# Optimization experiments

Measured on AMD Instinct MI355X. Metric: run time of the kernel, lower is better.

## Reference

```python
import jax, jax.numpy as jnp
import numpy as np

EPS = 1e-5


def _conv3x3(x, w):
    # x: [B,C,H,W], w: [O,I,3,3], stride 1, padding 1
    return jax.lax.conv_general_dilated(
        x, w, window_strides=(1, 1), padding=((1, 1), (1, 1)),
        dimension_numbers=("NCHW", "OIHW", "NCHW"))


def _bn(x, g, b, m, v):
    # inference-mode BatchNorm2d over channel dim
    inv = jax.lax.rsqrt(v + EPS) * g
    return x * inv[None, :, None, None] + (b - m * inv)[None, :, None, None]


def setup_inputs() -> dict:
    key = jax.random.key(0)
    B, C, H, W = 32, 256, 56, 56
    ks = jax.random.split(key, 16)
    x = jax.random.normal(ks[0], (B, C, H, W), dtype=jnp.float32)
    mask = (jax.random.uniform(ks[1], (B, 1, H, W)) < 0.5).astype(jnp.float32)
    # dilated mask = 3x3 max-pool of mask
    mask_dilate = jax.lax.reduce_window(
        mask, -jnp.inf, jax.lax.max, (1, 1, 3, 3), (1, 1, 1, 1), "SAME")
    mask_dilate = jnp.maximum(mask_dilate, 0.0).astype(jnp.float32)
    vector = (jax.random.uniform(ks[2], (B, C)) < 0.5).astype(jnp.float32)
    conv1_w = jax.random.normal(ks[3], (C, C, 3, 3), dtype=jnp.float32) * 0.05
    conv2_w = jax.random.normal(ks[4], (C, C, 3, 3), dtype=jnp.float32) * 0.05
    bn1_g = 1.0 + 0.1 * jax.random.normal(ks[5], (C,), dtype=jnp.float32)
    bn1_b = 0.1 * jax.random.normal(ks[6], (C,), dtype=jnp.float32)
    bn1_m = 0.1 * jax.random.normal(ks[7], (C,), dtype=jnp.float32)
    bn1_v = 0.5 + jax.random.uniform(ks[8], (C,), dtype=jnp.float32)
    bn2_g = 1.0 + 0.1 * jax.random.normal(ks[9], (C,), dtype=jnp.float32)
    bn2_b = 0.1 * jax.random.normal(ks[10], (C,), dtype=jnp.float32)
    bn2_m = 0.1 * jax.random.normal(ks[11], (C,), dtype=jnp.float32)
    bn2_v = 0.5 + jax.random.uniform(ks[12], (C,), dtype=jnp.float32)
    return dict(x=x, mask=mask, mask_dilate=mask_dilate, vector=vector,
                conv1_w=conv1_w, bn1_g=bn1_g, bn1_b=bn1_b, bn1_m=bn1_m, bn1_v=bn1_v,
                conv2_w=conv2_w, bn2_g=bn2_g, bn2_b=bn2_b, bn2_m=bn2_m, bn2_v=bn2_v)


def reference(x, mask, mask_dilate, vector,
              conv1_w, bn1_g, bn1_b, bn1_m, bn1_v,
              conv2_w, bn2_g, bn2_b, bn2_m, bn2_v):
    # Sparse BasicBlock, stride=1, no downsample, input_mask=True.
    identity = x
    h = x * mask_dilate                      # apply_mask(x, mask_dilate)
    h = _conv3x3(h, conv1_w) * mask          # conv3x3_mask(conv1, ...)
    h = jax.nn.relu(_bn(h, bn1_g, bn1_b, bn1_m, bn1_v)) * mask_dilate  # bn_relu_mask(bn1, relu, ., mask_dilate)
    h = h * mask                             # apply_mask(x, mask)
    h = h * vector[:, :, None, None]         # channel_process(x, vector)
    h = _conv3x3(h, conv2_w) * mask          # conv3x3_mask(conv2, ...)
    h = _bn(h, bn2_g, bn2_b, bn2_m, bn2_v) * mask  # bn_relu_mask(bn2, None, ., mask)
    out = identity + h * mask                # identity + apply_mask(x, mask)
    return jax.nn.relu(out)
```

## Files before the change

### kernel.cpp

```cpp
#include <hip/hip_runtime.h>
#include <cstdint>


#define EPS 1e-5f

constexpr int Bn = 32, Cc = 256, Hh = 56, Ww = 56;
constexpr int HW = Hh * Ww;
constexpr int PD = 58;
constexpr int PP = PD * PD;
constexpr int SLAB = PP * 8;
constexpr int IMG_ELEMS = 32 * SLAB;
constexpr int WP_ELEMS = 2 * 16 * 9 * 2 * 128 * 8;

typedef __bf16 bf16x8 __attribute__((ext_vector_type(8)));
typedef float  f32x16 __attribute__((ext_vector_type(16)));

__global__ void pack_xm(const float* __restrict__ x, const float* __restrict__ md,
                        __bf16* __restrict__ xm) {
    int prow = blockIdx.x, img = blockIdx.y;
    int gy = prow - 1;
    bool rv = (unsigned)gy < 56u;
    for (int u = threadIdx.x; u < 32 * 64; u += 256) {
        int cg = u >> 6, pcol = u & 63;
        if (pcol >= PD) continue;
        int gx = pcol - 1;
        bf16x8 v = {};
        if (rv && (unsigned)gx < 56u) {
            float mdv = md[img * HW + gy * 56 + gx];
            const float* xp = x + ((size_t)img * Cc + cg * 8) * HW + gy * 56 + gx;
            #pragma unroll
            for (int j = 0; j < 8; ++j)
                v[j] = (__bf16)(xp[(size_t)j * HW] * mdv);
        }
        *(bf16x8*)&xm[(size_t)(img * 32 + cg) * SLAB + (prow * PD + pcol) * 8] = v;
    }
}

__global__ void cmap_kern(const float* __restrict__ vec, int* __restrict__ act,
                          int* __restrict__ inv, int* __restrict__ meta) {
    int img = threadIdx.x;
    if (img >= Bn) return;
    int n = 0;
    for (int c = 0; c < Cc; ++c) {
        if (vec[img * Cc + c] != 0.f) { act[img * Cc + n] = c; inv[img * Cc + c] = n; ++n; }
        else inv[img * Cc + c] = -1;
    }
    for (int k = n; k < Cc; ++k) act[img * Cc + k] = 0;
    meta[img] = n;
    meta[Bn + img] = (n + 15) >> 4;
}

__global__ void zero_u(__bf16* __restrict__ u, const int* __restrict__ meta) {
    int img = blockIdx.x;
    int nact = meta[img], nch = meta[Bn + img];
    __bf16* base = u + (size_t)img * IMG_ELEMS;
    bf16x8 z = {};
    int nslab = 2 * nch;
    for (int s = 0; s < nslab; ++s) {
        __bf16* sb = base + (size_t)s * SLAB;
        if (8 * s + 7 >= nact) {
            for (int t = threadIdx.x; t < PP; t += 256)
                *(bf16x8*)&sb[t * 8] = z;
        } else {
            for (int t = threadIdx.x; t < 228; t += 256) {
                int prow, pcol;
                if (t < 58)       { prow = 0;        pcol = t; }
                else if (t < 116) { prow = 57;       pcol = t - 58; }
                else if (t < 172) { prow = t - 115;  pcol = 0; }
                else              { prow = t - 171;  pcol = 57; }
                *(bf16x8*)&sb[(prow * PD + pcol) * 8] = z;
            }
        }
    }
}

__global__ void pack_w1(const float* __restrict__ w1, __bf16* __restrict__ wp1) {
    int id = blockIdx.x * 256 + threadIdx.x;
    int j = id & 7; int t = id >> 3;
    int col = t & 127; t >>= 7;
    int half = t & 1; t >>= 1;
    int tap = t % 9; t /= 9;
    int chunk = t & 15; int coblk = t >> 4;
    int co = coblk * 128 + col;
    int ci = chunk * 16 + half * 8 + j;
    wp1[id] = (__bf16)(w1[((size_t)co * Cc + ci) * 9 + tap]);
}

__global__ void gather_w2(const float* __restrict__ w2, const int* __restrict__ act,
                          const int* __restrict__ meta, __bf16* __restrict__ wp2g) {
    int img = blockIdx.y;
    int id = blockIdx.x * 256 + threadIdx.x;
    int nact = meta[img], nch = meta[Bn + img];
    int j = id & 7; int t = id >> 3;
    int col = t & 127; t >>= 7;
    int half = t & 1; t >>= 1;
    int tap = t % 9; t /= 9;
    int chunk = t & 15; int coblk = t >> 4;
    if (chunk >= nch) return;
    int kslot = chunk * 16 + half * 8 + j;
    float v = 0.f;
    if (kslot < nact) {
        int co = coblk * 128 + col;
        v = w2[((size_t)co * Cc + act[img * Cc + kslot]) * 9 + tap];
    }
    wp2g[(size_t)img * WP_ELEMS + id] = (__bf16)v;
}

__global__ void bn_prep(const float* g1, const float* b1, const float* m1, const float* v1,
                        const float* g2, const float* b2, const float* m2, const float* v2,
                        float* binv1, float* bbeta1, float* binv2, float* bbeta2) {
    int c = threadIdx.x;
    float i1 = g1[c] * rsqrtf(v1[c] + EPS);
    binv1[c] = i1; bbeta1[c] = b1[c] - m1[c] * i1;
    float i2 = g2[c] * rsqrtf(v2[c] + EPS);
    binv2[c] = i2; bbeta2[c] = b2[c] - m2[c] * i2;
}

__device__ __forceinline__ void gl_lds16(const __bf16* g, __bf16* l) {
    __builtin_amdgcn_global_load_lds(
        (const __attribute__((address_space(1))) void*)g,
        (__attribute__((address_space(3))) void*)l, 16, 0, 0);
}

template <bool C1>
__global__ __launch_bounds__(256, 3)
void conv_kern(const __bf16* __restrict__ src,
               const __bf16* __restrict__ wp,
               const float* __restrict__ maskg,
               const float* __restrict__ vec,
               const int* __restrict__ inv,
               const int* __restrict__ meta,
               const float* __restrict__ binv, const float* __restrict__ bbeta,
               const float* __restrict__ xin,
               void* __restrict__ dstv) {
    constexpr int SINB = 2 * 4 * 66 * 8;
    constexpr int SWB  = 9 * 2 * 128 * 8;
    __shared__ __align__(16) __bf16 s_in[SINB];
    __shared__ __align__(16) __bf16 s_w[SWB];

    const int tid = threadIdx.x;
    const int lane = tid & 63, wave = tid >> 6;
    const int xlane = lane & 31, halfid = lane >> 5;
    const int pxg = wave >> 1, cog = wave & 1;

    const int bid = blockIdx.x;
    const int wg = (bid & 7) * 224 + (bid >> 3);
    const int img = wg / 56;
    const int t = wg - img * 56;
    const int y0 = (t >> 1) * 2;
    const int coblk = t & 1;
    const int co0c = coblk * 128;

    const int nloop = C1 ? 16 : meta[Bn + img];

    f32x16 acc[2][2];
    #pragma unroll
    for (int a = 0; a < 2; ++a)
        #pragma unroll
        for (int b = 0; b < 2; ++b)
            #pragma unroll
            for (int r = 0; r < 16; ++r) acc[a][b][r] = 0.f;

    const __bf16* wblk = C1 ? (wp + (size_t)coblk * (16 * SWB))
                            : (wp + (size_t)img * WP_ELEMS + (size_t)coblk * (16 * SWB));
    const float* maskp = maskg + (size_t)img * HW;
    const __bf16* srcimg = src + (size_t)img * IMG_ELEMS;

    auto STAGE_IN = [&](int chunk) {
        const __bf16* slab = srcimg + (size_t)chunk * (2 * SLAB);
        #pragma unroll
        for (int k = 0; k < 3; ++k) {
            int u0 = wave * 64 + k * 256;
            int u = u0 + lane;
            if (u < 528) {
                int half = u / 264, rem = u - half * 264;
                int row = rem / 66, xx = rem - row * 66;
                int pcol = xx < PD ? xx : PD - 1;
                gl_lds16(slab + ((size_t)half * SLAB) + ((y0 + row) * PD + pcol) * 8,
                         &s_in[u0 * 8]);
            }
        }
    };
    auto STAGE_W = [&](int chunk) {
        const __bf16* g = wblk + (size_t)chunk * SWB;
        #pragma unroll
        for (int k = 0; k < 9; ++k) {
            int u0 = wave * 64 + k * 256;
            gl_lds16(g + (size_t)(u0 + lane) * 8, &s_w[u0 * 8]);
        }
    };

    for (int c = 0; c < nloop; ++c) {
        STAGE_W(c);
        STAGE_IN(c);
        asm volatile("s_waitcnt vmcnt(0)" ::: "memory");
        __builtin_amdgcn_sched_barrier(0);
        __builtin_amdgcn_s_barrier();
        __builtin_amdgcn_sched_barrier(0);

        __builtin_amdgcn_s_setprio(1);
        #pragma unroll
        for (int kh = 0; kh < 3; ++kh)
            #pragma unroll
            for (int kw = 0; kw < 3; ++kw) {
                const int tap = kh * 3 + kw;
                bf16x8 wf[2], inf[2];
                #pragma unroll
                for (int jt = 0; jt < 2; ++jt)
                    wf[jt] = *(const bf16x8*)&s_w[((tap * 2 + halfid) * 128 +
                                                   (cog * 2 + jt) * 32 + xlane) * 8];
                #pragma unroll
                for (int it = 0; it < 2; ++it) {
                    int yy = pxg + kh;
                    int xx = it * 32 + xlane + kw;
                    inf[it] = *(const bf16x8*)&s_in[((halfid * 4 + yy) * 66 + xx) * 8];
                }
                #pragma unroll
                for (int it = 0; it < 2; ++it)
                    #pragma unroll
                    for (int jt = 0; jt < 2; ++jt) {
                        if constexpr (C1)
                            acc[it][jt] = __builtin_amdgcn_mfma_f32_32x32x16_bf16(
                                inf[it], wf[jt], acc[it][jt], 0, 0, 0);
                        else
                            acc[it][jt] = __builtin_amdgcn_mfma_f32_32x32x16_bf16(
                                wf[jt], inf[it], acc[it][jt], 0, 0, 0);
                    }
            }
        __builtin_amdgcn_s_setprio(0);
        __builtin_amdgcn_sched_barrier(0);
        __builtin_amdgcn_s_barrier();
        __builtin_amdgcn_sched_barrier(0);
    }

    const int y = y0 + pxg;
    if constexpr (C1) {
        __bf16* u = (__bf16*)dstv;
        float iv[2], bt[2], vv[2]; int slt[2]; size_t slb[2];
        #pragma unroll
        for (int jt = 0; jt < 2; ++jt) {
            int co = co0c + (cog * 2 + jt) * 32 + xlane;
            iv[jt] = binv[co];
            bt[jt] = bbeta[co];
            vv[jt] = vec[img * Cc + co];
            slt[jt] = inv[img * Cc + co];
            int s = slt[jt] < 0 ? 0 : slt[jt];
            slb[jt] = (size_t)(img * 32 + (s >> 3)) * SLAB + (s & 7);
        }
        #pragma unroll
        for (int it = 0; it < 2; ++it) {
            int xb = it * 32;
            #pragma unroll
            for (int reg = 0; reg < 16; ++reg) {
                int x = xb + (reg & 3) + 8 * (reg >> 2) + 4 * halfid;
                if (x < 56) {
                    float mv = maskp[y * 56 + x];
                    int poff = ((y + 1) * PD + (x + 1)) * 8;
                    #pragma unroll
                    for (int jt = 0; jt < 2; ++jt) {
                        if (slt[jt] >= 0) {
                            float o = fmaxf(fmaf(acc[it][jt][reg], iv[jt], bt[jt]), 0.f)
                                      * mv * vv[jt];
                            u[slb[jt] + poff] = (__bf16)o;
                        }
                    }
                }
            }
        }
    } else {
        float* outp = (float*)dstv;
        int xa[2]; float mva[2]; bool ok[2];
        #pragma unroll
        for (int it = 0; it < 2; ++it) {
            xa[it] = it * 32 + xlane;
            ok[it] = xa[it] < 56;
            mva[it] = ok[it] ? maskp[y * 56 + xa[it]] : 0.f;
        }
        #pragma unroll
        for (int jt = 0; jt < 2; ++jt) {
            int cb = co0c + (cog * 2 + jt) * 32;
            #pragma unroll
            for (int rg = 0; rg < 4; ++rg) {
                int c4 = cb + 8 * rg + 4 * halfid;
                float4 iv4 = *(const float4*)&binv[c4];
                float4 bt4 = *(const float4*)&bbeta[c4];
                float ivv[4] = {iv4.x, iv4.y, iv4.z, iv4.w};
                float btv[4] = {bt4.x, bt4.y, bt4.z, bt4.w};
                #pragma unroll
                for (int j = 0; j < 4; ++j) {
                    int reg = rg * 4 + j;
                    int co = c4 + j;
                    size_t cbase = (size_t)(img * Cc + co) * HW;
                    #pragma unroll
                    for (int it = 0; it < 2; ++it) {
                        if (ok[it]) {
                            size_t oa = cbase + y * 56 + xa[it];
                            float ov = fmaxf(
                                xin[oa] + mva[it] * fmaf(acc[it][jt][reg], ivv[j], btv[j]),
                                0.f);
                            outp[oa] = ov;
                        }
                    }
                }
            }
        }
    }
}

extern "C" void kernel_launch(void* const* d_in, const int* in_sizes, int n_in,
                              void* d_out, int out_size, void* d_ws, size_t ws_size,
                              hipStream_t stream) {
    const float* x    = (const float*)d_in[0];
    const float* mask = (const float*)d_in[1];
    const float* md   = (const float*)d_in[2];
    const float* vec  = (const float*)d_in[3];
    const float* w1   = (const float*)d_in[4];
    const float* bn1g = (const float*)d_in[5];
    const float* bn1b = (const float*)d_in[6];
    const float* bn1m = (const float*)d_in[7];
    const float* bn1v = (const float*)d_in[8];
    const float* w2   = (const float*)d_in[9];
    const float* bn2g = (const float*)d_in[10];
    const float* bn2b = (const float*)d_in[11];
    const float* bn2m = (const float*)d_in[12];
    const float* bn2v = (const float*)d_in[13];
    float* out = (float*)d_out;

    const size_t npad = (size_t)Bn * IMG_ELEMS;
    __bf16* xm  = (__bf16*)d_ws;
    __bf16* u   = xm + npad;
    __bf16* wp1 = u + npad;
    int* act    = (int*)(wp1 + WP_ELEMS);
    int* invm   = act + Bn * Cc;
    int* meta   = invm + Bn * Cc;
    float* binv1  = (float*)(meta + 64);
    float* bbeta1 = binv1 + 256;
    float* binv2  = bbeta1 + 256;
    float* bbeta2 = binv2 + 256;
    __bf16* wp2g = xm;

    pack_xm<<<dim3(PD, Bn), dim3(256), 0, stream>>>(x, md, xm);
    pack_w1<<<dim3(WP_ELEMS / 256), dim3(256), 0, stream>>>(w1, wp1);
    cmap_kern<<<dim3(1), dim3(64), 0, stream>>>(vec, act, invm, meta);
    zero_u<<<dim3(Bn), dim3(256), 0, stream>>>(u, meta);
    bn_prep<<<dim3(1), dim3(256), 0, stream>>>(bn1g, bn1b, bn1m, bn1v,
                                               bn2g, bn2b, bn2m, bn2v,
                                               binv1, bbeta1, binv2, bbeta2);

    conv_kern<true><<<dim3(1792), dim3(256), 0, stream>>>(
        xm, wp1, mask, vec, invm, meta, binv1, bbeta1, nullptr, u);
    gather_w2<<<dim3(WP_ELEMS / 256, Bn), dim3(256), 0, stream>>>(w2, act, meta, wp2g);
    conv_kern<false><<<dim3(1792), dim3(256), 0, stream>>>(
        u, wp2g, mask, nullptr, invm, meta, binv2, bbeta2, x, out);
}
```

Measured before the change: 569.0 us.

## Skip inactive output channels in conv1 via per-image gathered weights

Conv1 now computes only the output channels that are active in the channel vector. A new per-image gather packs the active channels' weights into compact slots, and a block whose 128-channel tile is entirely inactive exits early, so with about half the channels active roughly half the conv1 blocks skip their MFMA work. Conv2's weight gather reads from a pre-transposed bf16 copy and writes vectorized 8-element chunks, and the channel-map kernel uses wavefront ballots across one block per image. In exchange there are extra gather and transpose kernels, the output buffer is used as scratch for the gathered conv1 weights, and per-image weight reads replace shared ones, which can lower cache reuse.

```diff
diff --git a/kernel.cpp b/kernel.cpp
--- a/kernel.cpp
+++ b/kernel.cpp
@@ -37,17 +37,21 @@
 }
 
 __global__ void cmap_kern(const float* __restrict__ vec, int* __restrict__ act,
-                          int* __restrict__ inv, int* __restrict__ meta) {
-    int img = threadIdx.x;
-    if (img >= Bn) return;
-    int n = 0;
-    for (int c = 0; c < Cc; ++c) {
-        if (vec[img * Cc + c] != 0.f) { act[img * Cc + n] = c; inv[img * Cc + c] = n; ++n; }
-        else inv[img * Cc + c] = -1;
-    }
-    for (int k = n; k < Cc; ++k) act[img * Cc + k] = 0;
-    meta[img] = n;
-    meta[Bn + img] = (n + 15) >> 4;
+                          int* __restrict__ meta) {
+    int img = blockIdx.x, lane = threadIdx.x;
+    int base = 0;
+    #pragma unroll
+    for (int g = 0; g < 4; ++g) {
+        int c = g * 64 + lane;
+        bool a = vec[img * Cc + c] != 0.f;
+        unsigned long long m = __ballot(a);
+        int pos = __popcll(m & ((1ull << lane) - 1ull));
+        if (a) act[img * Cc + base + pos] = c;
+        base += (int)__popcll(m);
+    }
+    __syncthreads();
+    for (int k = base + lane; k < Cc; k += 64) act[img * Cc + k] = 0;
+    if (lane == 0) { meta[img] = base; meta[Bn + img] = (base + 15) >> 4; }
 }
 
 __global__ void zero_u(__bf16* __restrict__ u, const int* __restrict__ meta) {
@@ -86,24 +90,57 @@
     wp1[id] = (__bf16)(w1[((size_t)co * Cc + ci) * 9 + tap]);
 }
 
-__global__ void gather_w2(const float* __restrict__ w2, const int* __restrict__ act,
-                          const int* __restrict__ meta, __bf16* __restrict__ wp2g) {
+__global__ void pack_w2T(const float* __restrict__ w2, __bf16* __restrict__ wpT) {
+    int id = blockIdx.x * 256 + threadIdx.x;
+    int co = id & 255; int t = id >> 8;
+    int tap = t % 9; int ci = t / 9;
+    wpT[id] = (__bf16)(w2[((size_t)co * Cc + ci) * 9 + tap]);
+}
+
+__global__ void gather_w1(const __bf16* __restrict__ wp1, const int* __restrict__ act,
+                          const int* __restrict__ meta, __bf16* __restrict__ wp1g) {
     int img = blockIdx.y;
-    int id = blockIdx.x * 256 + threadIdx.x;
-    int nact = meta[img], nch = meta[Bn + img];
-    int j = id & 7; int t = id >> 3;
-    int col = t & 127; t >>= 7;
+    int uidx = blockIdx.x * 256 + threadIdx.x;
+    int nact = meta[img];
+    int col = uidx & 127; int t = uidx >> 7;
     int half = t & 1; t >>= 1;
     int tap = t % 9; t /= 9;
     int chunk = t & 15; int coblk = t >> 4;
+    if (coblk * 128 >= nact) return;
+    int slot = coblk * 128 + col;
+    bf16x8 v = {};
+    if (slot < nact) {
+        int co = act[img * Cc + slot];
+        v = *(const bf16x8*)&wp1[(size_t)(((((co >> 7) * 16 + chunk) * 9 + tap) * 2 + half)
+                                          * 128 + (co & 127)) * 8];
+    }
+    *(bf16x8*)&wp1g[(size_t)img * WP_ELEMS + (size_t)uidx * 8] = v;
+}
+
+__global__ void gather_w2(const __bf16* __restrict__ wpT, const int* __restrict__ act,
+                          const int* __restrict__ meta, __bf16* __restrict__ wp2g) {
+    int img = blockIdx.y;
+    int blk = blockIdx.x;
+    int coblk = blk >> 4, chunk = blk & 15;
+    int nact = meta[img], nch = meta[Bn + img];
     if (chunk >= nch) return;
-    int kslot = chunk * 16 + half * 8 + j;
-    float v = 0.f;
-    if (kslot < nact) {
-        int co = coblk * 128 + col;
-        v = w2[((size_t)co * Cc + act[img * Cc + kslot]) * 9 + tap];
-    }
-    wp2g[(size_t)img * WP_ELEMS + id] = (__bf16)v;
+    int half = threadIdx.x >> 7, co = threadIdx.x & 127;
+    int cog = coblk * 128 + co;
+    int ci8[8];
+    #pragma unroll
+    for (int j = 0; j < 8; ++j) {
+        int ks = chunk * 16 + half * 8 + j;
+        ci8[j] = ks < nact ? act[img * Cc + ks] : -1;
+    }
+    #pragma unroll
+    for (int tap = 0; tap < 9; ++tap) {
+        bf16x8 v;
+        #pragma unroll
+        for (int j = 0; j < 8; ++j)
+            v[j] = ci8[j] >= 0 ? wpT[(size_t)(ci8[j] * 9 + tap) * 256 + cog] : (__bf16)0.f;
+        *(bf16x8*)&wp2g[(size_t)img * WP_ELEMS +
+                        (size_t)((((coblk * 16 + chunk) * 9 + tap) * 2 + half) * 128 + co) * 8] = v;
+    }
 }
 
 __global__ void bn_prep(const float* g1, const float* b1, const float* m1, const float* v1,
@@ -127,8 +164,7 @@
 void conv_kern(const __bf16* __restrict__ src,
                const __bf16* __restrict__ wp,
                const float* __restrict__ maskg,
-               const float* __restrict__ vec,
-               const int* __restrict__ inv,
+               const int* __restrict__ act,
                const int* __restrict__ meta,
                const float* __restrict__ binv, const float* __restrict__ bbeta,
                const float* __restrict__ xin,
@@ -151,6 +187,8 @@
     const int coblk = t & 1;
     const int co0c = coblk * 128;
 
+    const int nact = meta[img];
+    if constexpr (C1) { if (co0c >= nact) return; }
     const int nloop = C1 ? 16 : meta[Bn + img];
 
     f32x16 acc[2][2];
@@ -161,8 +199,7 @@
             #pragma unroll
             for (int r = 0; r < 16; ++r) acc[a][b][r] = 0.f;
 
-    const __bf16* wblk = C1 ? (wp + (size_t)coblk * (16 * SWB))
-                            : (wp + (size_t)img * WP_ELEMS + (size_t)coblk * (16 * SWB));
+    const __bf16* wblk = wp + (size_t)img * WP_ELEMS + (size_t)coblk * (16 * SWB);
     const float* maskp = maskg + (size_t)img * HW;
     const __bf16* srcimg = src + (size_t)img * IMG_ELEMS;
 
@@ -236,16 +273,15 @@
     const int y = y0 + pxg;
     if constexpr (C1) {
         __bf16* u = (__bf16*)dstv;
-        float iv[2], bt[2], vv[2]; int slt[2]; size_t slb[2];
+        float iv[2], bt[2]; bool on[2]; size_t slb[2];
         #pragma unroll
         for (int jt = 0; jt < 2; ++jt) {
-            int co = co0c + (cog * 2 + jt) * 32 + xlane;
-            iv[jt] = binv[co];
-            bt[jt] = bbeta[co];
-            vv[jt] = vec[img * Cc + co];
-            slt[jt] = inv[img * Cc + co];
-            int s = slt[jt] < 0 ? 0 : slt[jt];
-            slb[jt] = (size_t)(img * 32 + (s >> 3)) * SLAB + (s & 7);
+            int slt = co0c + (cog * 2 + jt) * 32 + xlane;
+            on[jt] = slt < nact;
+            int ch = on[jt] ? act[img * Cc + slt] : 0;
+            iv[jt] = binv[ch];
+            bt[jt] = bbeta[ch];
+            slb[jt] = (size_t)(img * 32 + (slt >> 3)) * SLAB + (slt & 7);
         }
         #pragma unroll
         for (int it = 0; it < 2; ++it) {
@@ -258,9 +294,8 @@
                     int poff = ((y + 1) * PD + (x + 1)) * 8;
                     #pragma unroll
                     for (int jt = 0; jt < 2; ++jt) {
-                        if (slt[jt] >= 0) {
-                            float o = fmaxf(fmaf(acc[it][jt][reg], iv[jt], bt[jt]), 0.f)
-                                      * mv * vv[jt];
+                        if (on[jt]) {
+                            float o = fmaxf(fmaf(acc[it][jt][reg], iv[jt], bt[jt]), 0.f) * mv;
                             u[slb[jt] + poff] = (__bf16)o;
                         }
                     }
@@ -330,26 +365,29 @@
     __bf16* xm  = (__bf16*)d_ws;
     __bf16* u   = xm + npad;
     __bf16* wp1 = u + npad;
-    int* act    = (int*)(wp1 + WP_ELEMS);
-    int* invm   = act + Bn * Cc;
-    int* meta   = invm + Bn * Cc;
+    __bf16* wpT = wp1 + WP_ELEMS;
+    int* act    = (int*)(wpT + WP_ELEMS);
+    int* meta   = act + Bn * Cc;
     float* binv1  = (float*)(meta + 64);
     float* bbeta1 = binv1 + 256;
     float* binv2  = bbeta1 + 256;
     float* bbeta2 = binv2 + 256;
     __bf16* wp2g = xm;
+    __bf16* wp1g = (__bf16*)d_out;
 
     pack_xm<<<dim3(PD, Bn), dim3(256), 0, stream>>>(x, md, xm);
     pack_w1<<<dim3(WP_ELEMS / 256), dim3(256), 0, stream>>>(w1, wp1);
-    cmap_kern<<<dim3(1), dim3(64), 0, stream>>>(vec, act, invm, meta);
+    pack_w2T<<<dim3(WP_ELEMS / 256), dim3(256), 0, stream>>>(w2, wpT);
+    cmap_kern<<<dim3(Bn), dim3(64), 0, stream>>>(vec, act, meta);
     zero_u<<<dim3(Bn), dim3(256), 0, stream>>>(u, meta);
     bn_prep<<<dim3(1), dim3(256), 0, stream>>>(bn1g, bn1b, bn1m, bn1v,
                                                bn2g, bn2b, bn2m, bn2v,
                                                binv1, bbeta1, binv2, bbeta2);
+    gather_w1<<<dim3(288, Bn), dim3(256), 0, stream>>>(wp1, act, meta, wp1g);
 
     conv_kern<true><<<dim3(1792), dim3(256), 0, stream>>>(
-        xm, wp1, mask, vec, invm, meta, binv1, bbeta1, nullptr, u);
-    gather_w2<<<dim3(WP_ELEMS / 256, Bn), dim3(256), 0, stream>>>(w2, act, meta, wp2g);
+        xm, wp1g, mask, act, meta, binv1, bbeta1, nullptr, u);
+    gather_w2<<<dim3(32, Bn), dim3(256), 0, stream>>>(wpT, act, meta, wp2g);
     conv_kern<false><<<dim3(1792), dim3(256), 0, stream>>>(
-        u, wp2g, mask, nullptr, invm, meta, binv2, bbeta2, x, out);
-}
+        u, wp2g, mask, act, meta, binv2, bbeta2, x, out);
+}
```

Result: faster. 503.0 us (-11.6%).
